# Optimization experiments

Measured on AMD Instinct MI355X. Metric: run time of the kernel, lower is better.

The kernel has to match this reference:

```python
import jax, jax.numpy as jnp
import numpy as np

NUM_KERNELS = 301
GAMMA = 10.0
SHIFT = float(np.log(2.0))


def shifted_softplus(x):
    return jax.nn.softplus(x) - SHIFT


def setup_inputs() -> dict:
    key = jax.random.key(0)
    k1, k2, k3, k4, k5, k6 = jax.random.split(key, 6)
    N, F, K = 768, 128, NUM_KERNELS
    x = jax.random.normal(k1, (N, F), dtype=jnp.float32)
    # positions scaled to span a realistic distance range vs centers in [0, 30]
    r = jax.random.uniform(k2, (N, 3), dtype=jnp.float32) * 10.0
    W1 = jax.random.normal(k3, (K, F), dtype=jnp.float32) * (1.0 / np.sqrt(K))
    b1 = jax.random.normal(k4, (F,), dtype=jnp.float32) * 0.01
    W2 = jax.random.normal(k5, (F, F), dtype=jnp.float32) * (1.0 / np.sqrt(F))
    b2 = jax.random.normal(k6, (F,), dtype=jnp.float32) * 0.01
    return {"x": x, "r": r, "W1": W1, "b1": b1, "W2": W2, "b2": b2}


def reference(x, r, W1, b1, W2, b2):
    # pairwise Euclidean distances, safe at the zero diagonal
    diff = r[:, None, :] - r[None, :, :]            # [N, N, 3]
    sq = jnp.sum(diff * diff, axis=-1)              # [N, N]
    d = jnp.where(sq > 0, jnp.sqrt(jnp.where(sq > 0, sq, 1.0)), 0.0)
    centers = jnp.linspace(0.0, 30.0, NUM_KERNELS, dtype=jnp.float32)  # [K]
    expanded = jnp.exp(-GAMMA * jnp.square(d[..., None] - centers))    # [N, N, K]
    h = shifted_softplus(expanded @ W1 + b1)        # [N, N, F]
    w = shifted_softplus(h @ W2 + b2)               # [N, N, F]
    o = jnp.einsum('jk,ijk->ik', x, w)              # [N, F]
    return o
```

## Files before the change

kernel.cpp:

```cpp
#include <hip/hip_runtime.h>

#define F        128
#define NN       768
#define KE       192
#define E_STRIDE 56
#define H_STRIDE 136
#define NT       48
#define NBLK     (NT*(NT+1)/2)

#define L2E 1.44269504f
#define LN2 0.69314718f
#define DQS 3782.0f
#define DQI (1.0f/3782.0f)

typedef __attribute__((ext_vector_type(8))) short short8;
typedef __attribute__((ext_vector_type(4))) float floatx4;

__device__ __forceinline__ unsigned short f2bf(float f) {
    union { float f; unsigned u; } v; v.f = f;
    return (unsigned short)((v.u + 0x8000u) >> 16);
}

__device__ __forceinline__ unsigned cvt_pk_bf16(float lo, float hi) {
    unsigned r;
    asm("v_cvt_pk_bf16_f32 %0, %1, %2" : "=v"(r) : "v"(lo), "v"(hi));
    return r;
}

__device__ __forceinline__ float ssp_l2(float zl2e) {
    float t = exp2f(zl2e);
    float u = __log2f(1.0f + t);
    return fmaf(LN2, u, -LN2);
}

__device__ __forceinline__ void pin(short8& v) { asm volatile("" : "+v"(v)); }

__device__ __forceinline__ void bar_lds() {
    asm volatile("s_waitcnt lgkmcnt(0)" ::: "memory");
    __builtin_amdgcn_s_barrier();
}

__device__ __forceinline__ int klo_from_d(float d) {
    int k = (int)ceilf(fmaf(10.0f, d, -13.0f));
    k &= ~1;
    return k < 0 ? 0 : (k > KE - 32 ? KE - 32 : k);
}

__global__ void prep_w(const float* __restrict__ W1, const float* __restrict__ W2,
                       unsigned short* __restrict__ W1s, unsigned short* __restrict__ W2s,
                       float* __restrict__ out) {
    int idx = blockIdx.x * 256 + threadIdx.x;
    out[idx] = 0.0f;
    if (idx < KE * F) {
        int t = idx & 7, lane = (idx >> 3) & 63, frag = idx >> 9;
        int k = (frag >> 3) * 32 + (lane >> 4) * 8 + t;
        int n = (frag & 7) * 16 + (lane & 15);
        W1s[idx] = f2bf(W1[k * F + n] * L2E);
    } else if (idx < KE * F + F * F) {
        int j = idx - KE * F;
        int t = j & 7, lane = (j >> 3) & 63, frag = j >> 9;
        int k = (frag >> 3) * 32 + (lane >> 4) * 8 + t;
        int n = (frag & 7) * 16 + (lane & 15);
        W2s[j] = f2bf(W2[k * F + n] * L2E);
    }
}

__global__ __launch_bounds__(256, 2) void cfconv_main(
    const float* __restrict__ x, const float* __restrict__ r,
    const float* __restrict__ b1, const float* __restrict__ b2,
    const unsigned short* __restrict__ W1s, const unsigned short* __restrict__ W2s,
    float* __restrict__ out)
{
    __shared__ __align__(16) unsigned short e_lds[64 * E_STRIDE];
    __shared__ __align__(16) unsigned short h_lds[64 * H_STRIDE];
    __shared__ unsigned short d_all[256];
    __shared__ unsigned short klo8_lds[64];

    const int tid  = threadIdx.x;
    const int lane = tid & 63;
    const int wave = tid >> 6;
    const int quad = lane >> 4;
    const int l15  = lane & 15;

    int b = blockIdx.x;
    int A = (int)((97.0f - sqrtf(9409.0f - 8.0f * (float)b)) * 0.5f);
    while ((A + 1) * (97 - (A + 1)) / 2 <= b) ++A;
    while (A * (97 - A) / 2 > b) --A;
    const int B = A + (b - A * (97 - A) / 2);
    const int Ai0 = A * 16, Bj0 = B * 16;
    const bool diag = (A == B);

    short8 w1f[6][2], w2f[4][2];
    #pragma unroll
    for (int ks = 0; ks < KE / 32; ++ks) {
        w1f[ks][0] = *(const short8*)&W1s[((ks*8 + wave*2 + 0) * 64 + lane) * 8];
        w1f[ks][1] = *(const short8*)&W1s[((ks*8 + wave*2 + 1) * 64 + lane) * 8];
    }
    #pragma unroll
    for (int ks = 0; ks < F / 32; ++ks) {
        w2f[ks][0] = *(const short8*)&W2s[((ks*8 + wave*2 + 0) * 64 + lane) * 8];
        w2f[ks][1] = *(const short8*)&W2s[((ks*8 + wave*2 + 1) * 64 + lane) * 8];
    }
    #pragma unroll
    for (int ks = 0; ks < 6; ++ks) { pin(w1f[ks][0]); pin(w1f[ks][1]); }
    #pragma unroll
    for (int ks = 0; ks < 4; ++ks) { pin(w2f[ks][0]); pin(w2f[ks][1]); }

    {
        int p = tid;
        int gi = Ai0 + (p >> 4), gj = Bj0 + (p & 15);
        float dx = r[gi*3+0] - r[gj*3+0];
        float dy = r[gi*3+1] - r[gj*3+1];
        float dz = r[gi*3+2] - r[gj*3+2];
        float sq = dx*dx + dy*dy + dz*dz;
        float d  = sq > 0.0f ? sqrtf(sq) : 0.0f;
        d_all[p] = (unsigned short)fmaf(d, DQS, 0.5f);
    }

    const int c0 = wave * 32 + l15;
    const int c1 = c0 + 16;
    const float b1L0 = b1[c0] * L2E, b1L1 = b1[c1] * L2E;
    const float b2L0 = b2[c0] * L2E, b2L1 = b2[c1] * L2E;

    float xB0[4], xB1[4];
    #pragma unroll
    for (int rg = 0; rg < 4; ++rg) {
        int gj = Bj0 + quad * 4 + rg;
        xB0[rg] = x[gj * F + c0];
        xB1[rg] = x[gj * F + c1];
    }
    float oB0[4] = {0,0,0,0}, oB1[4] = {0,0,0,0};

    const int rq16 = 16 * ((l15 >> 2) & 3);

    bar_lds();

    for (int s = 0; s < 4; ++s) {
        {
            int row = tid >> 2;
            int lo4 = tid & 3;
            float d = (float)d_all[s * 64 + row] * DQI;
            int klo8 = klo_from_d(d) & ~7;
            if (lo4 == 0) klo8_lds[row] = (unsigned short)klo8;
            #pragma unroll
            for (int pass = 0; pass < 12; ++pass) {
                int loc = lo4 + pass * 4;
                float t = fmaf(-0.1f, (float)(klo8 + loc), d);
                float e = exp2f(t * t * (-10.0f * L2E));
                e_lds[row * E_STRIDE + loc] = f2bf(e);
            }
        }
        bar_lds();

        floatx4 acc[4][2];
        {
            floatx4 bi0 = {b1L0, b1L0, b1L0, b1L0};
            floatx4 bi1 = {b1L1, b1L1, b1L1, b1L1};
            #pragma unroll
            for (int mt = 0; mt < 4; ++mt) { acc[mt][0] = bi0; acc[mt][1] = bi1; }
        }
        int klo8r[4];
        #pragma unroll
        for (int mt = 0; mt < 4; ++mt) klo8r[mt] = klo8_lds[mt*16 + l15];
        __builtin_amdgcn_s_setprio(1);
        #pragma unroll
        for (int ks = 0; ks < KE / 32; ++ks) {
            short8 af[4];
            #pragma unroll
            for (int mt = 0; mt < 4; ++mt) {
                int off = ks*32 + quad*8 - klo8r[mt];
                off = ((unsigned)off > 32u) ? 40 : off;
                af[mt] = *(const short8*)&e_lds[(mt*16 + l15) * E_STRIDE + off];
            }
            #pragma unroll
            for (int mt = 0; mt < 4; ++mt) {
                acc[mt][0] = __builtin_amdgcn_mfma_f32_16x16x32_bf16(af[mt], w1f[ks][0], acc[mt][0], 0, 0, 0);
                acc[mt][1] = __builtin_amdgcn_mfma_f32_16x16x32_bf16(af[mt], w1f[ks][1], acc[mt][1], 0, 0, 0);
            }
        }
        __builtin_amdgcn_s_setprio(0);

        #pragma unroll
        for (int mt = 0; mt < 4; ++mt) {
            #pragma unroll
            for (int rg = 0; rg < 4; ++rg) {
                int row = mt*16 + quad*4 + rg;
                float h0 = ssp_l2(acc[mt][0][rg]);
                float h1 = ssp_l2(acc[mt][1][rg]);
                unsigned pk = cvt_pk_bf16(h0, h1);
                h_lds[row * H_STRIDE + ((c0 + 16*quad) & 127)] = (unsigned short)pk;
                h_lds[row * H_STRIDE + ((c1 + 16*quad) & 127)] = (unsigned short)(pk >> 16);
            }
        }
        bar_lds();

        float xA0[4], xA1[4];
        #pragma unroll
        for (int mt = 0; mt < 4; ++mt) {
            int gi = Ai0 + s*4 + mt;
            xA0[mt] = x[gi * F + c0];
            xA1[mt] = x[gi * F + c1];
        }

        floatx4 acc2[4][2];
        {
            floatx4 bi0 = {b2L0, b2L0, b2L0, b2L0};
            floatx4 bi1 = {b2L1, b2L1, b2L1, b2L1};
            #pragma unroll
            for (int mt = 0; mt < 4; ++mt) { acc2[mt][0] = bi0; acc2[mt][1] = bi1; }
        }
        __builtin_amdgcn_s_setprio(1);
        #pragma unroll
        for (int ks = 0; ks < F / 32; ++ks) {
            int ko = (ks*32 + quad*8 + rq16) & 127;
            short8 af[4];
            #pragma unroll
            for (int mt = 0; mt < 4; ++mt)
                af[mt] = *(const short8*)&h_lds[(mt*16 + l15) * H_STRIDE + ko];
            #pragma unroll
            for (int mt = 0; mt < 4; ++mt) {
                acc2[mt][0] = __builtin_amdgcn_mfma_f32_16x16x32_bf16(af[mt], w2f[ks][0], acc2[mt][0], 0, 0, 0);
                acc2[mt][1] = __builtin_amdgcn_mfma_f32_16x16x32_bf16(af[mt], w2f[ks][1], acc2[mt][1], 0, 0, 0);
            }
        }
        __builtin_amdgcn_s_setprio(0);

        float oA0[4] = {0,0,0,0}, oA1[4] = {0,0,0,0};
        #pragma unroll
        for (int mt = 0; mt < 4; ++mt) {
            #pragma unroll
            for (int rg = 0; rg < 4; ++rg) {
                float w0 = ssp_l2(acc2[mt][0][rg]);
                float w1 = ssp_l2(acc2[mt][1][rg]);
                oA0[mt] = fmaf(xB0[rg], w0, oA0[mt]);
                oA1[mt] = fmaf(xB1[rg], w1, oA1[mt]);
                if (!diag) {
                    oB0[rg] = fmaf(xA0[mt], w0, oB0[rg]);
                    oB1[rg] = fmaf(xA1[mt], w1, oB1[rg]);
                }
            }
        }
        #pragma unroll
        for (int mt = 0; mt < 4; ++mt) {
            oA0[mt] += __shfl_xor(oA0[mt], 16, 64); oA0[mt] += __shfl_xor(oA0[mt], 32, 64);
            oA1[mt] += __shfl_xor(oA1[mt], 16, 64); oA1[mt] += __shfl_xor(oA1[mt], 32, 64);
        }
        if (lane < 16) {
            #pragma unroll
            for (int mt = 0; mt < 4; ++mt) {
                int gi = Ai0 + s*4 + mt;
                atomicAdd(&out[gi * F + c0], oA0[mt]);
                atomicAdd(&out[gi * F + c1], oA1[mt]);
            }
        }
    }

    if (!diag) {
        #pragma unroll
        for (int rg = 0; rg < 4; ++rg) {
            int gj = Bj0 + quad * 4 + rg;
            atomicAdd(&out[gj * F + c0], oB0[rg]);
            atomicAdd(&out[gj * F + c1], oB1[rg]);
        }
    }
}

extern "C" void kernel_launch(void* const* d_in, const int* in_sizes, int n_in,
                              void* d_out, int out_size, void* d_ws, size_t ws_size,
                              hipStream_t stream) {
    const float* x  = (const float*)d_in[0];
    const float* r  = (const float*)d_in[1];
    const float* W1 = (const float*)d_in[2];
    const float* b1 = (const float*)d_in[3];
    const float* W2 = (const float*)d_in[4];
    const float* b2 = (const float*)d_in[5];
    float* out = (float*)d_out;

    unsigned short* W1s = (unsigned short*)d_ws;
    unsigned short* W2s = W1s + KE * F;

    prep_w<<<(NN * F) / 256, 256, 0, stream>>>(W1, W2, W1s, W2s, out);
    cfconv_main<<<NBLK, 256, 0, stream>>>(x, r, b1, b2, W1s, W2s, out);
}
```

Baseline: 124.0 us.

## Split each pair tile's four row sub-tiles into separate blocks

Removes the per-block loop over four 4-row sub-tiles and launches one block per sub-tile, quadrupling the grid. Distances are now kept in float rather than 16-bit quantised, and Gaussian features are written as packed bf16 pairs. This aims to improve latency hiding and load balance across CUs. In exchange, weight fragments are reloaded per block and B-side atomics increase fourfold.

Result: faster. 119.3 us (-3.7%).

```diff
diff --git a/kernel.cpp b/kernel.cpp
--- a/kernel.cpp
+++ b/kernel.cpp
@@ -6,12 +6,11 @@
 #define E_STRIDE 56
 #define H_STRIDE 136
 #define NT       48
-#define NBLK     (NT*(NT+1)/2)
+#define NPAIR    (NT*(NT+1)/2)
+#define NBLK     (NPAIR*4)
 
 #define L2E 1.44269504f
 #define LN2 0.69314718f
-#define DQS 3782.0f
-#define DQI (1.0f/3782.0f)
 
 typedef __attribute__((ext_vector_type(8))) short short8;
 typedef __attribute__((ext_vector_type(4))) float floatx4;
@@ -73,7 +72,7 @@
 {
     __shared__ __align__(16) unsigned short e_lds[64 * E_STRIDE];
     __shared__ __align__(16) unsigned short h_lds[64 * H_STRIDE];
-    __shared__ unsigned short d_all[256];
+    __shared__ float d_all[64];
     __shared__ unsigned short klo8_lds[64];
 
     const int tid  = threadIdx.x;
@@ -82,7 +81,9 @@
     const int quad = lane >> 4;
     const int l15  = lane & 15;
 
-    int b = blockIdx.x;
+    int bidx = blockIdx.x;
+    const int s = bidx & 3;
+    int b = bidx >> 2;
     int A = (int)((97.0f - sqrtf(9409.0f - 8.0f * (float)b)) * 0.5f);
     while ((A + 1) * (97 - (A + 1)) / 2 <= b) ++A;
     while (A * (97 - A) / 2 > b) --A;
@@ -106,15 +107,13 @@
     #pragma unroll
     for (int ks = 0; ks < 4; ++ks) { pin(w2f[ks][0]); pin(w2f[ks][1]); }
 
-    {
-        int p = tid;
-        int gi = Ai0 + (p >> 4), gj = Bj0 + (p & 15);
+    if (tid < 64) {
+        int gi = Ai0 + s * 4 + (tid >> 4), gj = Bj0 + (tid & 15);
         float dx = r[gi*3+0] - r[gj*3+0];
         float dy = r[gi*3+1] - r[gj*3+1];
         float dz = r[gi*3+2] - r[gj*3+2];
         float sq = dx*dx + dy*dy + dz*dz;
-        float d  = sq > 0.0f ? sqrtf(sq) : 0.0f;
-        d_all[p] = (unsigned short)fmaf(d, DQS, 0.5f);
+        d_all[tid] = sq > 0.0f ? sqrtf(sq) : 0.0f;
     }
 
     const int c0 = wave * 32 + l15;
@@ -122,6 +121,13 @@
     const float b1L0 = b1[c0] * L2E, b1L1 = b1[c1] * L2E;
     const float b2L0 = b2[c0] * L2E, b2L1 = b2[c1] * L2E;
 
+    float xA0[4], xA1[4];
+    #pragma unroll
+    for (int mt = 0; mt < 4; ++mt) {
+        int gi = Ai0 + s*4 + mt;
+        xA0[mt] = x[gi * F + c0];
+        xA1[mt] = x[gi * F + c1];
+    }
     float xB0[4], xB1[4];
     #pragma unroll
     for (int rg = 0; rg < 4; ++rg) {
@@ -129,132 +135,124 @@
         xB0[rg] = x[gj * F + c0];
         xB1[rg] = x[gj * F + c1];
     }
+
+    const int rq16 = 16 * ((l15 >> 2) & 3);
+
+    bar_lds();
+
+    {
+        int row = tid >> 2;
+        int lo4 = tid & 3;
+        float d = d_all[row];
+        int klo8 = klo_from_d(d) & ~7;
+        if (lo4 == 0) klo8_lds[row] = (unsigned short)klo8;
+        unsigned* e32 = (unsigned*)&e_lds[row * E_STRIDE];
+        #pragma unroll
+        for (int pass = 0; pass < 6; ++pass) {
+            int loc = lo4 * 2 + pass * 8;
+            float t0 = fmaf(-0.1f, (float)(klo8 + loc), d);
+            float t1 = fmaf(-0.1f, (float)(klo8 + loc + 1), d);
+            float e0 = exp2f(t0 * t0 * (-10.0f * L2E));
+            float e1 = exp2f(t1 * t1 * (-10.0f * L2E));
+            e32[loc >> 1] = cvt_pk_bf16(e0, e1);
+        }
+    }
+    bar_lds();
+
+    floatx4 acc[4][2];
+    {
+        floatx4 bi0 = {b1L0, b1L0, b1L0, b1L0};
+        floatx4 bi1 = {b1L1, b1L1, b1L1, b1L1};
+        #pragma unroll
+        for (int mt = 0; mt < 4; ++mt) { acc[mt][0] = bi0; acc[mt][1] = bi1; }
+    }
+    int klo8r[4];
+    #pragma unroll
+    for (int mt = 0; mt < 4; ++mt) klo8r[mt] = klo8_lds[mt*16 + l15];
+    __builtin_amdgcn_s_setprio(1);
+    #pragma unroll
+    for (int ks = 0; ks < KE / 32; ++ks) {
+        short8 af[4];
+        #pragma unroll
+        for (int mt = 0; mt < 4; ++mt) {
+            int off = ks*32 + quad*8 - klo8r[mt];
+            off = ((unsigned)off > 32u) ? 40 : off;
+            af[mt] = *(const short8*)&e_lds[(mt*16 + l15) * E_STRIDE + off];
+        }
+        #pragma unroll
+        for (int mt = 0; mt < 4; ++mt) {
+            acc[mt][0] = __builtin_amdgcn_mfma_f32_16x16x32_bf16(af[mt], w1f[ks][0], acc[mt][0], 0, 0, 0);
+            acc[mt][1] = __builtin_amdgcn_mfma_f32_16x16x32_bf16(af[mt], w1f[ks][1], acc[mt][1], 0, 0, 0);
+        }
+    }
+    __builtin_amdgcn_s_setprio(0);
+
+    #pragma unroll
+    for (int mt = 0; mt < 4; ++mt) {
+        #pragma unroll
+        for (int rg = 0; rg < 4; ++rg) {
+            int row = mt*16 + quad*4 + rg;
+            float h0 = ssp_l2(acc[mt][0][rg]);
+            float h1 = ssp_l2(acc[mt][1][rg]);
+            unsigned pk = cvt_pk_bf16(h0, h1);
+            h_lds[row * H_STRIDE + ((c0 + 16*quad) & 127)] = (unsigned short)pk;
+            h_lds[row * H_STRIDE + ((c1 + 16*quad) & 127)] = (unsigned short)(pk >> 16);
+        }
+    }
+    bar_lds();
+
+    floatx4 acc2[4][2];
+    {
+        floatx4 bi0 = {b2L0, b2L0, b2L0, b2L0};
+        floatx4 bi1 = {b2L1, b2L1, b2L1, b2L1};
+        #pragma unroll
+        for (int mt = 0; mt < 4; ++mt) { acc2[mt][0] = bi0; acc2[mt][1] = bi1; }
+    }
+    __builtin_amdgcn_s_setprio(1);
+    #pragma unroll
+    for (int ks = 0; ks < F / 32; ++ks) {
+        int ko = (ks*32 + quad*8 + rq16) & 127;
+        short8 af[4];
+        #pragma unroll
+        for (int mt = 0; mt < 4; ++mt)
+            af[mt] = *(const short8*)&h_lds[(mt*16 + l15) * H_STRIDE + ko];
+        #pragma unroll
+        for (int mt = 0; mt < 4; ++mt) {
+            acc2[mt][0] = __builtin_amdgcn_mfma_f32_16x16x32_bf16(af[mt], w2f[ks][0], acc2[mt][0], 0, 0, 0);
+            acc2[mt][1] = __builtin_amdgcn_mfma_f32_16x16x32_bf16(af[mt], w2f[ks][1], acc2[mt][1], 0, 0, 0);
+        }
+    }
+    __builtin_amdgcn_s_setprio(0);
+
+    float oA0[4] = {0,0,0,0}, oA1[4] = {0,0,0,0};
     float oB0[4] = {0,0,0,0}, oB1[4] = {0,0,0,0};
-
-    const int rq16 = 16 * ((l15 >> 2) & 3);
-
-    bar_lds();
-
-    for (int s = 0; s < 4; ++s) {
-        {
-            int row = tid >> 2;
-            int lo4 = tid & 3;
-            float d = (float)d_all[s * 64 + row] * DQI;
-            int klo8 = klo_from_d(d) & ~7;
-            if (lo4 == 0) klo8_lds[row] = (unsigned short)klo8;
-            #pragma unroll
-            for (int pass = 0; pass < 12; ++pass) {
-                int loc = lo4 + pass * 4;
-                float t = fmaf(-0.1f, (float)(klo8 + loc), d);
-                float e = exp2f(t * t * (-10.0f * L2E));
-                e_lds[row * E_STRIDE + loc] = f2bf(e);
+    #pragma unroll
+    for (int mt = 0; mt < 4; ++mt) {
+        #pragma unroll
+        for (int rg = 0; rg < 4; ++rg) {
+            float w0 = ssp_l2(acc2[mt][0][rg]);
+            float w1 = ssp_l2(acc2[mt][1][rg]);
+            oA0[mt] = fmaf(xB0[rg], w0, oA0[mt]);
+            oA1[mt] = fmaf(xB1[rg], w1, oA1[mt]);
+            if (!diag) {
+                oB0[rg] = fmaf(xA0[mt], w0, oB0[rg]);
+                oB1[rg] = fmaf(xA1[mt], w1, oB1[rg]);
             }
         }
-        bar_lds();
-
-        floatx4 acc[4][2];
-        {
-            floatx4 bi0 = {b1L0, b1L0, b1L0, b1L0};
-            floatx4 bi1 = {b1L1, b1L1, b1L1, b1L1};
-            #pragma unroll
-            for (int mt = 0; mt < 4; ++mt) { acc[mt][0] = bi0; acc[mt][1] = bi1; }
-        }
-        int klo8r[4];
-        #pragma unroll
-        for (int mt = 0; mt < 4; ++mt) klo8r[mt] = klo8_lds[mt*16 + l15];
-        __builtin_amdgcn_s_setprio(1);
-        #pragma unroll
-        for (int ks = 0; ks < KE / 32; ++ks) {
-            short8 af[4];
-            #pragma unroll
-            for (int mt = 0; mt < 4; ++mt) {
-                int off = ks*32 + quad*8 - klo8r[mt];
-                off = ((unsigned)off > 32u) ? 40 : off;
-                af[mt] = *(const short8*)&e_lds[(mt*16 + l15) * E_STRIDE + off];
-            }
-            #pragma unroll
-            for (int mt = 0; mt < 4; ++mt) {
-                acc[mt][0] = __builtin_amdgcn_mfma_f32_16x16x32_bf16(af[mt], w1f[ks][0], acc[mt][0], 0, 0, 0);
-                acc[mt][1] = __builtin_amdgcn_mfma_f32_16x16x32_bf16(af[mt], w1f[ks][1], acc[mt][1], 0, 0, 0);
-            }
-        }
-        __builtin_amdgcn_s_setprio(0);
-
-        #pragma unroll
-        for (int mt = 0; mt < 4; ++mt) {
-            #pragma unroll
-            for (int rg = 0; rg < 4; ++rg) {
-                int row = mt*16 + quad*4 + rg;
-                float h0 = ssp_l2(acc[mt][0][rg]);
-                float h1 = ssp_l2(acc[mt][1][rg]);
-                unsigned pk = cvt_pk_bf16(h0, h1);
-                h_lds[row * H_STRIDE + ((c0 + 16*quad) & 127)] = (unsigned short)pk;
-                h_lds[row * H_STRIDE + ((c1 + 16*quad) & 127)] = (unsigned short)(pk >> 16);
-            }
-        }
-        bar_lds();
-
-        float xA0[4], xA1[4];
+    }
+    #pragma unroll
+    for (int mt = 0; mt < 4; ++mt) {
+        oA0[mt] += __shfl_xor(oA0[mt], 16, 64); oA0[mt] += __shfl_xor(oA0[mt], 32, 64);
+        oA1[mt] += __shfl_xor(oA1[mt], 16, 64); oA1[mt] += __shfl_xor(oA1[mt], 32, 64);
+    }
+    if (lane < 16) {
         #pragma unroll
         for (int mt = 0; mt < 4; ++mt) {
             int gi = Ai0 + s*4 + mt;
-            xA0[mt] = x[gi * F + c0];
-            xA1[mt] = x[gi * F + c1];
-        }
-
-        floatx4 acc2[4][2];
-        {
-            floatx4 bi0 = {b2L0, b2L0, b2L0, b2L0};
-            floatx4 bi1 = {b2L1, b2L1, b2L1, b2L1};
-            #pragma unroll
-            for (int mt = 0; mt < 4; ++mt) { acc2[mt][0] = bi0; acc2[mt][1] = bi1; }
-        }
-        __builtin_amdgcn_s_setprio(1);
-        #pragma unroll
-        for (int ks = 0; ks < F / 32; ++ks) {
-            int ko = (ks*32 + quad*8 + rq16) & 127;
-            short8 af[4];
-            #pragma unroll
-            for (int mt = 0; mt < 4; ++mt)
-                af[mt] = *(const short8*)&h_lds[(mt*16 + l15) * H_STRIDE + ko];
-            #pragma unroll
-            for (int mt = 0; mt < 4; ++mt) {
-                acc2[mt][0] = __builtin_amdgcn_mfma_f32_16x16x32_bf16(af[mt], w2f[ks][0], acc2[mt][0], 0, 0, 0);
-                acc2[mt][1] = __builtin_amdgcn_mfma_f32_16x16x32_bf16(af[mt], w2f[ks][1], acc2[mt][1], 0, 0, 0);
-            }
-        }
-        __builtin_amdgcn_s_setprio(0);
-
-        float oA0[4] = {0,0,0,0}, oA1[4] = {0,0,0,0};
-        #pragma unroll
-        for (int mt = 0; mt < 4; ++mt) {
-            #pragma unroll
-            for (int rg = 0; rg < 4; ++rg) {
-                float w0 = ssp_l2(acc2[mt][0][rg]);
-                float w1 = ssp_l2(acc2[mt][1][rg]);
-                oA0[mt] = fmaf(xB0[rg], w0, oA0[mt]);
-                oA1[mt] = fmaf(xB1[rg], w1, oA1[mt]);
-                if (!diag) {
-                    oB0[rg] = fmaf(xA0[mt], w0, oB0[rg]);
-                    oB1[rg] = fmaf(xA1[mt], w1, oB1[rg]);
-                }
-            }
-        }
-        #pragma unroll
-        for (int mt = 0; mt < 4; ++mt) {
-            oA0[mt] += __shfl_xor(oA0[mt], 16, 64); oA0[mt] += __shfl_xor(oA0[mt], 32, 64);
-            oA1[mt] += __shfl_xor(oA1[mt], 16, 64); oA1[mt] += __shfl_xor(oA1[mt], 32, 64);
-        }
-        if (lane < 16) {
-            #pragma unroll
-            for (int mt = 0; mt < 4; ++mt) {
-                int gi = Ai0 + s*4 + mt;
-                atomicAdd(&out[gi * F + c0], oA0[mt]);
-                atomicAdd(&out[gi * F + c1], oA1[mt]);
-            }
-        }
-    }
-
+            atomicAdd(&out[gi * F + c0], oA0[mt]);
+            atomicAdd(&out[gi * F + c1], oA1[mt]);
+        }
+    }
     if (!diag) {
         #pragma unroll
         for (int rg = 0; rg < 4; ++rg) {
```
